# Kernel tuning notes

Measured on AMD Instinct MI355X. Metric: run time of the kernel, lower is better.

The kernel has to match this reference:

```python
import math
import jax, jax.numpy as jnp
import numpy as np

B, T, C = 2, 2048, 1024
NH = 16
HS = C // NH
WIN = 256

def setup_inputs() -> dict:
    key = jax.random.key(0)
    k1, k2, k3 = jax.random.split(key, 3)
    x = jax.random.normal(k1, (B, T, C), dtype=jnp.float32)
    # Linear weights stored as (in, out) so y = x @ W
    scale_attn = 1.0 / math.sqrt(C)
    W_attn = jax.random.normal(k2, (C, 3 * C), dtype=jnp.float32) * scale_attn
    W_proj = jax.random.normal(k3, (C, C), dtype=jnp.float32) * scale_attn
    return {"x": x, "W_attn": W_attn, "W_proj": W_proj}

def reference(x, W_attn, W_proj):
    Bs, Ts, Cs = x.shape
    W = min(WIN, Ts)
    qkv = x @ W_attn                                  # [B,T,3C]
    q, k, v = jnp.split(qkv, 3, axis=-1)
    # [B,T,C] -> [B,NH,T,HS]
    q = q.reshape(Bs, Ts, NH, HS).transpose(0, 2, 1, 3)
    k = k.reshape(Bs, Ts, NH, HS).transpose(0, 2, 1, 3)
    v = v.reshape(Bs, Ts, NH, HS).transpose(0, 2, 1, 3)
    att = jnp.einsum('bhqd,bhkd->bhqk', q, k) * (1.0 / math.sqrt(HS))
    i_idx = jnp.arange(Ts)[:, None]
    j_idx = jnp.arange(Ts)[None, :]
    mask = (j_idx <= i_idx) & (i_idx - j_idx < W)      # causal sliding window
    att = jnp.where(mask[None, None, :, :], att, -jnp.inf)
    att = jax.nn.softmax(att, axis=-1)
    y = jnp.einsum('bhqk,bhkd->bhqd', att, v)          # [B,NH,T,HS]
    y = y.transpose(0, 2, 1, 3).reshape(Bs, Ts, Cs)
    return y @ W_proj
```

## Files before the change

### kernel.cpp

```cpp
#include <hip/hip_runtime.h>
#include <hip/hip_bf16.h>
#include <cstdint>

#define B_   2
#define T_   2048
#define C_   1024
#define NH_  16
#define HS_  64
#define WIN_ 256
#define M_   (B_*T_)

typedef __attribute__((ext_vector_type(8))) short          short8;
typedef __attribute__((ext_vector_type(8))) unsigned short ushortx8;
typedef __attribute__((ext_vector_type(8))) __bf16         bf16x8;
typedef __attribute__((ext_vector_type(4))) float          floatx4;

__device__ __forceinline__ unsigned short f2bf(float f) {
    union { float f; uint32_t u; } v; v.f = f;
    uint32_t r = (v.u + 0x7FFFu + ((v.u >> 16) & 1u)) >> 16;
    return (unsigned short)r;
}

__device__ __forceinline__ floatx4 mfma16(short8 a, short8 b, floatx4 c) {
    return __builtin_amdgcn_mfma_f32_16x16x32_bf16(
        __builtin_bit_cast(bf16x8, a), __builtin_bit_cast(bf16x8, b), c, 0, 0, 0);
}

__device__ __forceinline__ void async16(const void* g, void* l) {
    __builtin_amdgcn_global_load_lds(
        (const __attribute__((address_space(1))) void*)g,
        (__attribute__((address_space(3))) void*)l, 16, 0, 0);
}

__global__ __launch_bounds__(256)
void convert_bf16(const float* __restrict__ in, unsigned short* __restrict__ out)
{
    int i = (blockIdx.x * 256 + threadIdx.x) * 4;
    float4 v = *(const float4*)&in[i];
    ushort4 h;
    h.x = f2bf(v.x); h.y = f2bf(v.y); h.z = f2bf(v.z); h.w = f2bf(v.w);
    *(ushort4*)&out[i] = h;
}

__global__ __launch_bounds__(256)
void transpose_convert(const float* __restrict__ in, unsigned short* __restrict__ out,
                       int K, int N)
{
    __shared__ unsigned short tile[64][72];
    const int k0 = blockIdx.y * 64, n0 = blockIdx.x * 64;
    const int tr = threadIdx.x >> 4;
    const int tc = (threadIdx.x & 15) * 4;
    #pragma unroll
    for (int it = 0; it < 4; it++) {
        int row = tr + it * 16;
        float4 v = *(const float4*)&in[(size_t)(k0 + row) * N + n0 + tc];
        ushort4 h;
        h.x = f2bf(v.x); h.y = f2bf(v.y); h.z = f2bf(v.z); h.w = f2bf(v.w);
        *(ushort4*)&tile[row][tc] = h;
    }
    __syncthreads();
    #pragma unroll
    for (int it = 0; it < 4; it++) {
        int nrow = tr + it * 16;
        ushort4 h;
        h.x = tile[tc + 0][nrow]; h.y = tile[tc + 1][nrow];
        h.z = tile[tc + 2][nrow]; h.w = tile[tc + 3][nrow];
        *(ushort4*)&out[(size_t)(n0 + nrow) * K + k0 + tc] = h;
    }
}

template<bool OUT_BF16>
__global__ __launch_bounds__(256)
void gemm_bt(const unsigned short* __restrict__ A,
             const unsigned short* __restrict__ Bt,
             void* __restrict__ Cp, int M, int N, int K)
{
    constexpr int BK = 32;
    __shared__ unsigned short As[128 * BK];
    __shared__ unsigned short Bs[128 * BK];

    const int tid  = threadIdx.x;
    const int lane = tid & 63;
    const int wave = tid >> 6;
    const int l16  = lane & 15;
    const int quad = lane >> 4;
    const int wm   = (wave & 1) * 64;
    const int wn   = (wave >> 1) * 64;
    const int m0   = blockIdx.y * 128;
    const int n0   = blockIdx.x * 128;

    const int srow = wave * 16 + (lane >> 2);
    const int scol = (lane & 3) * 8;

    floatx4 acc[4][4];
    #pragma unroll
    for (int i = 0; i < 4; i++)
        #pragma unroll
        for (int j = 0; j < 4; j++) acc[i][j] = (floatx4){0.f, 0.f, 0.f, 0.f};

    const unsigned short* gA = &A[(size_t)(m0 + srow) * K + scol];
    const unsigned short* gB = &Bt[(size_t)(n0 + srow) * K + scol];
    unsigned short* lA = &As[wave * 16 * BK];
    unsigned short* lB = &Bs[wave * 16 * BK];

    for (int k0 = 0; k0 < K; k0 += BK) {
        async16(gA + k0,            lA);
        async16(gA + k0 + 64 * K,   lA + 64 * BK);
        async16(gB + k0,            lB);
        async16(gB + k0 + 64 * K,   lB + 64 * BK);
        __syncthreads();

        short8 af[4], bfr[4];
        #pragma unroll
        for (int i = 0; i < 4; i++)
            af[i] = *(const short8*)(&As[(wm + i * 16 + l16) * BK + quad * 8]);
        #pragma unroll
        for (int j = 0; j < 4; j++)
            bfr[j] = *(const short8*)(&Bs[(wn + j * 16 + l16) * BK + quad * 8]);
        #pragma unroll
        for (int i = 0; i < 4; i++)
            #pragma unroll
            for (int j = 0; j < 4; j++)
                acc[i][j] = mfma16(af[i], bfr[j], acc[i][j]);
        __syncthreads();
    }

    #pragma unroll
    for (int i = 0; i < 4; i++)
        #pragma unroll
        for (int j = 0; j < 4; j++)
            #pragma unroll
            for (int r = 0; r < 4; r++) {
                int row = m0 + wm + i * 16 + quad * 4 + r;
                int col = n0 + wn + j * 16 + l16;
                if (OUT_BF16)
                    ((unsigned short*)Cp)[(size_t)row * N + col] = f2bf(acc[i][j][r]);
                else
                    ((float*)Cp)[(size_t)row * N + col] = acc[i][j][r];
            }
}

__global__ __launch_bounds__(256)
void attn_kernel(const unsigned short* __restrict__ qkv, unsigned short* __restrict__ y)
{
    constexpr int PD = 72;
    __shared__ unsigned short Qs[64 * PD];
    __shared__ unsigned short Ks[64 * PD];
    __shared__ unsigned short Vt[64 * PD];
    __shared__ unsigned short Ps[4][16 * PD];

    const int tid  = threadIdx.x;
    const int lane = tid & 63;
    const int wave = tid >> 6;
    const int l16  = lane & 15;
    const int quad = lane >> 4;

    const int q0 = blockIdx.x * 64;
    const int h  = blockIdx.y;
    const int b  = blockIdx.z;
    const size_t base = (size_t)b * T_;
    const int ROW = 3 * C_;
    const int qoff = h * HS_;
    const int koff = C_ + h * HS_;
    const int voff = 2 * C_ + h * HS_;

    #pragma unroll
    for (int it = 0; it < 4; it++) {
        int c = tid + 256 * it;
        int row = c >> 4, dc = (c & 15) << 2;
        *(ushort4*)(&Qs[row * PD + dc]) =
            *(const ushort4*)(&qkv[(base + q0 + row) * ROW + qoff + dc]);
    }

    floatx4 O[4];
    #pragma unroll
    for (int j = 0; j < 4; j++) O[j] = (floatx4){0.f, 0.f, 0.f, 0.f};
    float m_i[4], l_i[4];
    #pragma unroll
    for (int r = 0; r < 4; r++) { m_i[r] = -1e30f; l_i[r] = 0.f; }

    const int kb_lo = (q0 - WIN_) > 0 ? (q0 - WIN_) : 0;
    for (int kb = kb_lo; kb <= q0; kb += 64) {
        __syncthreads();
        #pragma unroll
        for (int it = 0; it < 4; it++) {
            int c = tid + 256 * it;
            int row = c >> 4, dc = (c & 15) << 2;
            *(ushort4*)(&Ks[row * PD + dc]) =
                *(const ushort4*)(&qkv[(base + kb + row) * ROW + koff + dc]);
        }
        #pragma unroll
        for (int it = 0; it < 2; it++) {
            int c = tid + 256 * it;
            int row = c >> 3, db = (c & 7) * 8;
            ushortx8 v = *(const ushortx8*)&qkv[(base + kb + row) * ROW + voff + db];
            #pragma unroll
            for (int e = 0; e < 8; e++)
                Vt[(db + e) * PD + row] = v[e];
        }
        __syncthreads();

        floatx4 s[4];
        #pragma unroll
        for (int nt = 0; nt < 4; nt++) s[nt] = (floatx4){0.f, 0.f, 0.f, 0.f};
        #pragma unroll
        for (int ks = 0; ks < 2; ks++) {
            short8 a = *(const short8*)(&Qs[(wave * 16 + l16) * PD + ks * 32 + quad * 8]);
            #pragma unroll
            for (int nt = 0; nt < 4; nt++) {
                short8 bb = *(const short8*)(&Ks[(nt * 16 + l16) * PD + ks * 32 + quad * 8]);
                s[nt] = mfma16(a, bb, s[nt]);
            }
        }

        const int qrb = q0 + wave * 16 + quad * 4;
        float mt[4] = {-1e30f, -1e30f, -1e30f, -1e30f};
        #pragma unroll
        for (int nt = 0; nt < 4; nt++)
            #pragma unroll
            for (int r = 0; r < 4; r++) {
                int qa = qrb + r;
                int ka = kb + nt * 16 + l16;
                float val = s[nt][r] * 0.125f;
                bool ok = (ka <= qa) && (qa - ka < WIN_);
                val = ok ? val : -1e30f;
                s[nt][r] = val;
                mt[r] = fmaxf(mt[r], val);
            }
        #pragma unroll
        for (int r = 0; r < 4; r++) {
            #pragma unroll
            for (int off = 8; off >= 1; off >>= 1)
                mt[r] = fmaxf(mt[r], __shfl_xor(mt[r], off, 64));
        }

        float alpha[4];
        #pragma unroll
        for (int r = 0; r < 4; r++) {
            float mnew = fmaxf(m_i[r], mt[r]);
            alpha[r] = __expf(m_i[r] - mnew);
            m_i[r] = mnew;
        }
        float psum[4] = {0.f, 0.f, 0.f, 0.f};
        #pragma unroll
        for (int nt = 0; nt < 4; nt++)
            #pragma unroll
            for (int r = 0; r < 4; r++) {
                float p = (s[nt][r] > -1e29f) ? __expf(s[nt][r] - m_i[r]) : 0.f;
                s[nt][r] = p;
                psum[r] += p;
            }
        #pragma unroll
        for (int r = 0; r < 4; r++) {
            #pragma unroll
            for (int off = 8; off >= 1; off >>= 1)
                psum[r] += __shfl_xor(psum[r], off, 64);
            l_i[r] = l_i[r] * alpha[r] + psum[r];
        }
        #pragma unroll
        for (int jt = 0; jt < 4; jt++)
            #pragma unroll
            for (int r = 0; r < 4; r++) O[jt][r] *= alpha[r];

        #pragma unroll
        for (int nt = 0; nt < 4; nt++)
            #pragma unroll
            for (int r = 0; r < 4; r++)
                Ps[wave][(quad * 4 + r) * PD + nt * 16 + l16] = f2bf(s[nt][r]);

        #pragma unroll
        for (int ks = 0; ks < 2; ks++) {
            short8 a = *(const short8*)(&Ps[wave][l16 * PD + ks * 32 + quad * 8]);
            #pragma unroll
            for (int jt = 0; jt < 4; jt++) {
                short8 bb = *(const short8*)(&Vt[(jt * 16 + l16) * PD + ks * 32 + quad * 8]);
                O[jt] = mfma16(a, bb, O[jt]);
            }
        }
    }

    #pragma unroll
    for (int jt = 0; jt < 4; jt++)
        #pragma unroll
        for (int r = 0; r < 4; r++) {
            int qa = q0 + wave * 16 + quad * 4 + r;
            float o = O[jt][r] / l_i[r];
            y[(base + qa) * C_ + h * HS_ + jt * 16 + l16] = f2bf(o);
        }
}

extern "C" void kernel_launch(void* const* d_in, const int* in_sizes, int n_in,
                              void* d_out, int out_size, void* d_ws, size_t ws_size,
                              hipStream_t stream)
{
    const float* x      = (const float*)d_in[0];
    const float* W_attn = (const float*)d_in[1];
    const float* W_proj = (const float*)d_in[2];
    float* out = (float*)d_out;

    unsigned short* xb   = (unsigned short*)d_ws;
    unsigned short* Wa_t = xb   + (size_t)M_ * C_;
    unsigned short* Wp_t = Wa_t + (size_t)3 * C_ * C_;
    unsigned short* qkv  = Wp_t + (size_t)C_ * C_;
    unsigned short* y    = qkv  + (size_t)M_ * 3 * C_;

    dim3 blk(256);
    convert_bf16<<<(M_ * C_) / 1024, blk, 0, stream>>>(x, xb);
    transpose_convert<<<dim3((3 * C_) / 64, C_ / 64), blk, 0, stream>>>(W_attn, Wa_t, C_, 3 * C_);
    transpose_convert<<<dim3(C_ / 64, C_ / 64), blk, 0, stream>>>(W_proj, Wp_t, C_, C_);

    gemm_bt<true><<<dim3((3 * C_) / 128, M_ / 128), blk, 0, stream>>>(
        xb, Wa_t, qkv, M_, 3 * C_, C_);
    attn_kernel<<<dim3(T_ / 64, NH_, B_), blk, 0, stream>>>(qkv, y);
    gemm_bt<false><<<dim3(C_ / 128, M_ / 128), blk, 0, stream>>>(
        y, Wp_t, out, M_, C_, C_);
}
```

Baseline: 181.5 us.

## Merge prep kernels, pre-transpose V globally, and coalesce attention output stores

Folds the three fp32-to-bf16 conversion and transpose launches into one prep kernel that branches on block index. Adds a separate kernel that writes V in transposed [B,NH,HS,T] layout, so the attention loop loads V tiles with contiguous 16-byte copies instead of scattered per-element LDS writes. The attention epilogue stages normalized outputs in shared memory and writes them with vectorized row stores. The cost is an extra launch and a round trip of V through global memory, and it assumes the workspace has room for the new V buffer.

After: 186.4 us. 1.03x slower.

```diff
diff --git a/kernel.cpp b/kernel.cpp
--- a/kernel.cpp
+++ b/kernel.cpp
@@ -32,31 +32,24 @@
         (__attribute__((address_space(3))) void*)l, 16, 0, 0);
 }
 
-__global__ __launch_bounds__(256)
-void convert_bf16(const float* __restrict__ in, unsigned short* __restrict__ out)
-{
-    int i = (blockIdx.x * 256 + threadIdx.x) * 4;
-    float4 v = *(const float4*)&in[i];
-    ushort4 h;
-    h.x = f2bf(v.x); h.y = f2bf(v.y); h.z = f2bf(v.z); h.w = f2bf(v.w);
-    *(ushort4*)&out[i] = h;
-}
-
-__global__ __launch_bounds__(256)
-void transpose_convert(const float* __restrict__ in, unsigned short* __restrict__ out,
-                       int K, int N)
-{
-    __shared__ unsigned short tile[64][72];
-    const int k0 = blockIdx.y * 64, n0 = blockIdx.x * 64;
+#define NB_CONV 4096
+#define NB_WA   768
+#define NB_WP   256
+
+__device__ void transpose_tile(const float* __restrict__ in, unsigned short* __restrict__ out,
+                               int K, int N, int kt, int nt, unsigned short (*tile)[65])
+{
+    const int k0 = kt * 64, n0 = nt * 64;
     const int tr = threadIdx.x >> 4;
     const int tc = (threadIdx.x & 15) * 4;
     #pragma unroll
     for (int it = 0; it < 4; it++) {
         int row = tr + it * 16;
         float4 v = *(const float4*)&in[(size_t)(k0 + row) * N + n0 + tc];
-        ushort4 h;
-        h.x = f2bf(v.x); h.y = f2bf(v.y); h.z = f2bf(v.z); h.w = f2bf(v.w);
-        *(ushort4*)&tile[row][tc] = h;
+        tile[row][tc + 0] = f2bf(v.x);
+        tile[row][tc + 1] = f2bf(v.y);
+        tile[row][tc + 2] = f2bf(v.z);
+        tile[row][tc + 3] = f2bf(v.w);
     }
     __syncthreads();
     #pragma unroll
@@ -66,6 +59,58 @@
         h.x = tile[tc + 0][nrow]; h.y = tile[tc + 1][nrow];
         h.z = tile[tc + 2][nrow]; h.w = tile[tc + 3][nrow];
         *(ushort4*)&out[(size_t)(n0 + nrow) * K + k0 + tc] = h;
+    }
+}
+
+__global__ __launch_bounds__(256)
+void prep_kernel(const float* __restrict__ x, const float* __restrict__ W_attn,
+                 const float* __restrict__ W_proj,
+                 unsigned short* __restrict__ xb, unsigned short* __restrict__ Wa_t,
+                 unsigned short* __restrict__ Wp_t)
+{
+    __shared__ unsigned short tile[64][65];
+    const int bid = blockIdx.x;
+    if (bid < NB_CONV) {
+        int i = (bid * 256 + threadIdx.x) * 4;
+        float4 v = *(const float4*)&x[i];
+        ushort4 h;
+        h.x = f2bf(v.x); h.y = f2bf(v.y); h.z = f2bf(v.z); h.w = f2bf(v.w);
+        *(ushort4*)&xb[i] = h;
+    } else if (bid < NB_CONV + NB_WA) {
+        int idx = bid - NB_CONV;
+        transpose_tile(W_attn, Wa_t, C_, 3 * C_, idx / 48, idx % 48, tile);
+    } else {
+        int idx = bid - NB_CONV - NB_WA;
+        transpose_tile(W_proj, Wp_t, C_, C_, idx / 16, idx % 16, tile);
+    }
+}
+
+__global__ __launch_bounds__(256)
+void vtrans_kernel(const unsigned short* __restrict__ qkv, unsigned short* __restrict__ vt)
+{
+    __shared__ unsigned short tile[64][65];
+    const int t0 = blockIdx.x * 64;
+    const int h  = blockIdx.y;
+    const int b  = blockIdx.z;
+    const int tr = threadIdx.x >> 4;
+    const int tc = (threadIdx.x & 15) * 4;
+    const size_t inbase = ((size_t)b * T_) * (3 * C_) + 2 * C_ + h * 64;
+    #pragma unroll
+    for (int it = 0; it < 4; it++) {
+        int row = tr + it * 16;
+        ushort4 v = *(const ushort4*)&qkv[inbase + (size_t)(t0 + row) * (3 * C_) + tc];
+        tile[row][tc + 0] = v.x; tile[row][tc + 1] = v.y;
+        tile[row][tc + 2] = v.z; tile[row][tc + 3] = v.w;
+    }
+    __syncthreads();
+    const size_t outbase = ((size_t)(b * NH_ + h) * 64) * T_;
+    #pragma unroll
+    for (int it = 0; it < 4; it++) {
+        int d = tr + it * 16;
+        ushort4 h4;
+        h4.x = tile[tc + 0][d]; h4.y = tile[tc + 1][d];
+        h4.z = tile[tc + 2][d]; h4.w = tile[tc + 3][d];
+        *(ushort4*)&vt[outbase + (size_t)d * T_ + t0 + tc] = h4;
     }
 }
 
@@ -141,7 +186,9 @@
 }
 
 __global__ __launch_bounds__(256)
-void attn_kernel(const unsigned short* __restrict__ qkv, unsigned short* __restrict__ y)
+void attn_kernel(const unsigned short* __restrict__ qkv,
+                 const unsigned short* __restrict__ vt,
+                 unsigned short* __restrict__ y)
 {
     constexpr int PD = 72;
     __shared__ unsigned short Qs[64 * PD];
@@ -162,7 +209,7 @@
     const int ROW = 3 * C_;
     const int qoff = h * HS_;
     const int koff = C_ + h * HS_;
-    const int voff = 2 * C_ + h * HS_;
+    const size_t vbase = ((size_t)(b * NH_ + h) * 64) * T_;
 
     #pragma unroll
     for (int it = 0; it < 4; it++) {
@@ -192,11 +239,9 @@
         #pragma unroll
         for (int it = 0; it < 2; it++) {
             int c = tid + 256 * it;
-            int row = c >> 3, db = (c & 7) * 8;
-            ushortx8 v = *(const ushortx8*)&qkv[(base + kb + row) * ROW + voff + db];
-            #pragma unroll
-            for (int e = 0; e < 8; e++)
-                Vt[(db + e) * PD + row] = v[e];
+            int d = c >> 3, kc = (c & 7) * 8;
+            *(ushortx8*)(&Vt[d * PD + kc]) =
+                *(const ushortx8*)&vt[vbase + (size_t)d * T_ + kb + kc];
         }
         __syncthreads();
 
@@ -279,14 +324,22 @@
         }
     }
 
+    __syncthreads();
     #pragma unroll
     for (int jt = 0; jt < 4; jt++)
         #pragma unroll
         for (int r = 0; r < 4; r++) {
-            int qa = q0 + wave * 16 + quad * 4 + r;
-            float o = O[jt][r] / l_i[r];
-            y[(base + qa) * C_ + h * HS_ + jt * 16 + l16] = f2bf(o);
-        }
+            int ql = wave * 16 + quad * 4 + r;
+            Ks[ql * PD + jt * 16 + l16] = f2bf(O[jt][r] / l_i[r]);
+        }
+    __syncthreads();
+    #pragma unroll
+    for (int it = 0; it < 2; it++) {
+        int c = tid + 256 * it;
+        int qrow = c >> 3, dc = (c & 7) * 8;
+        *(ushortx8*)&y[(base + q0 + qrow) * C_ + h * HS_ + dc] =
+            *(const ushortx8*)(&Ks[qrow * PD + dc]);
+    }
 }
 
 extern "C" void kernel_launch(void* const* d_in, const int* in_sizes, int n_in,
@@ -303,15 +356,14 @@
     unsigned short* Wp_t = Wa_t + (size_t)3 * C_ * C_;
     unsigned short* qkv  = Wp_t + (size_t)C_ * C_;
     unsigned short* y    = qkv  + (size_t)M_ * 3 * C_;
+    unsigned short* vtg  = y    + (size_t)M_ * C_;
 
     dim3 blk(256);
-    convert_bf16<<<(M_ * C_) / 1024, blk, 0, stream>>>(x, xb);
-    transpose_convert<<<dim3((3 * C_) / 64, C_ / 64), blk, 0, stream>>>(W_attn, Wa_t, C_, 3 * C_);
-    transpose_convert<<<dim3(C_ / 64, C_ / 64), blk, 0, stream>>>(W_proj, Wp_t, C_, C_);
-
+    prep_kernel<<<NB_CONV + NB_WA + NB_WP, blk, 0, stream>>>(x, W_attn, W_proj, xb, Wa_t, Wp_t);
     gemm_bt<true><<<dim3((3 * C_) / 128, M_ / 128), blk, 0, stream>>>(
         xb, Wa_t, qkv, M_, 3 * C_, C_);
-    attn_kernel<<<dim3(T_ / 64, NH_, B_), blk, 0, stream>>>(qkv, y);
+    vtrans_kernel<<<dim3(T_ / 64, NH_, B_), blk, 0, stream>>>(qkv, vtg);
+    attn_kernel<<<dim3(T_ / 64, NH_, B_), blk, 0, stream>>>(qkv, vtg, y);
     gemm_bt<false><<<dim3(C_ / 128, M_ / 128), blk, 0, stream>>>(
         y, Wp_t, out, M_, C_, C_);
 }
```
